# Optimization experiments

Hardware: AMD Instinct MI355X
Metric: run time of the kernel (lower is better)

Reference implementation:

```python
import jax, jax.numpy as jnp
import numpy as np

B, C_IN, H, W = 4, 256, 256, 256
L = 5000                 # candidate lines per image
N_PTS0, N_PTS1 = 32, 8   # sampled points per line, pooled points
DIM_LOI, DIM_FC = 128, 1024
N_OUT_LINE = 2500


def setup_inputs() -> dict:
    key = jax.random.key(0)
    ks = jax.random.split(key, 8)
    feature = jax.random.normal(ks[0], (B, C_IN, H, W), jnp.float32)
    # line endpoints in [0, 255) pixel coords (row, col)
    lines_in = jax.random.uniform(ks[1], (B, L, 2, 2), jnp.float32) * 255.0
    fc1_w = jax.random.normal(ks[2], (DIM_LOI, C_IN), jnp.float32) * 0.05
    fc1_b = jnp.zeros((DIM_LOI,), jnp.float32)
    w1 = jax.random.normal(ks[3], (DIM_FC, DIM_LOI * N_PTS1), jnp.float32) * 0.02
    b1 = jnp.zeros((DIM_FC,), jnp.float32)
    w2 = jax.random.normal(ks[4], (DIM_FC, DIM_FC), jnp.float32) * 0.02
    b2 = jnp.zeros((DIM_FC,), jnp.float32)
    w3 = jax.random.normal(ks[5], (4, DIM_FC), jnp.float32) * 0.02
    b3 = jnp.zeros((4,), jnp.float32)
    return dict(feature=feature, lines_in=lines_in, fc1_w=fc1_w, fc1_b=fc1_b,
                w1=w1, b1=b1, w2=w2, b2=b2, w3=w3, b3=b3)


def _bilinear_sample(xi, px, py):
    # xi: [C, H, W]; px, py: [P] float coords. Matches torch clamp(0, 255).
    px0 = jnp.clip(jnp.floor(px), 0.0, 255.0)
    py0 = jnp.clip(jnp.floor(py), 0.0, 255.0)
    px1 = jnp.clip(px0 + 1.0, 0.0, 255.0)
    py1 = jnp.clip(py0 + 1.0, 0.0, 255.0)
    px0l, py0l = px0.astype(jnp.int32), py0.astype(jnp.int32)
    px1l, py1l = px1.astype(jnp.int32), py1.astype(jnp.int32)
    xp = (xi[:, px0l, py0l] * (px1 - px) * (py1 - py)
          + xi[:, px1l, py0l] * (px - px0) * (py1 - py)
          + xi[:, px0l, py1l] * (px1 - px) * (py - py0)
          + xi[:, px1l, py1l] * (px - px0) * (py - py0))
    return xp  # [C, P]


def _select(p0, s0, m):
    # p0: [L,2,2], s0: [L,4], m: [L] bool. Threshold-masked, argsort by argmax
    # class (descending), cyclically padded to N_OUT_LINE.
    max_idx = jnp.argmax(s0, axis=1)
    sort_key = jnp.where(m, max_idx, -1)          # unmasked rows sink to the end
    order = jnp.argsort(-sort_key)                # stable, descending by class id
    cnt = m.sum()
    idxs = jnp.arange(N_OUT_LINE) % jnp.maximum(cnt, 1)
    sel = order[idxs]
    li = jnp.where(cnt > 0, p0[sel], jnp.zeros_like(p0[sel]))
    si = jnp.where(cnt > 0, s0[sel], jnp.zeros_like(s0[sel]))
    return li, si


def reference(feature, lines_in, fc1_w, fc1_b, w1, b1, w2, b2, w3, b3):
    # fc1: 1x1 conv -> [B, DIM_LOI, H, W]
    x = jnp.einsum('bchw,oc->bohw', feature, fc1_w) + fc1_b[None, :, None, None]

    # sample N_PTS0 points along each line: p0*lam + p1*(1-lam) - 0.5
    lam = jnp.linspace(0.0, 1.0, N_PTS0, dtype=jnp.float32)[:, None]  # [32,1]
    pts = lines_in[:, :, 0:1, :] * lam + lines_in[:, :, 1:2, :] * (1.0 - lam) - 0.5  # [B,L,32,2]
    px = pts[..., 0].reshape(B, -1)  # [B, L*32]
    py = pts[..., 1].reshape(B, -1)

    xp = jax.vmap(_bilinear_sample)(x, px, py)            # [B, C, L*32]
    xp = xp.reshape(B, DIM_LOI, L, N_PTS0).transpose(0, 2, 1, 3)  # [B, L, C, 32]

    # MaxPool1d(4, 4) over the point axis -> [B, L, C, 8]
    xp = xp.reshape(B, L, DIM_LOI, N_PTS1, N_PTS0 // N_PTS1).max(axis=-1)
    flat = xp.reshape(B, L, DIM_LOI * N_PTS1)

    # fc2 MLP: 1024 -> 1024 -> 1024 -> 4
    h = jax.nn.relu(jnp.einsum('blf,df->bld', flat, w1) + b1)
    h = jax.nn.relu(jnp.einsum('bld,ed->ble', h, w2) + b2)
    logits = jnp.einsum('ble,oe->blo', h, w3) + b3        # [B, L, 4]

    s = jax.nn.softmax(logits, axis=-1)
    mask = ((s[..., 1] > 0.25) | (s[..., 2] > 0.25) | (s[..., 3] > 0.25)) & (s[..., 0] < 0.25)

    lines_out, score_out = jax.vmap(_select)(lines_in, s, mask)
    return lines_out, score_out  # [B, 2500, 2, 2], [B, 2500, 4]
```

## Files before the change

### kernel.cpp

```cpp
#include <hip/hip_runtime.h>
#include <hip/hip_bf16.h>
#include <math.h>

#define BB 4
#define C_IN 256
#define HH 256
#define WW 256
#define LL 5000
#define N_PTS0 32
#define N_PTS1 8
#define DIM_LOI 128
#define DIM_FC 1024
#define N_OUT_LINE 2500
#define MM (BB * LL)
#define PIX (HH * WW)

typedef __attribute__((ext_vector_type(8))) short short8_t;
typedef __attribute__((ext_vector_type(4))) float float4v;

__device__ __forceinline__ short f2bf(float f) {
    union { float f; unsigned u; } c; c.f = f;
    unsigned u = c.u;
    u += 0x7FFFu + ((u >> 16) & 1u);
    return (short)(u >> 16);
}
__device__ __forceinline__ float bf2f(short h) {
    union { unsigned u; float f; } c; c.u = ((unsigned)(unsigned short)h) << 16;
    return c.f;
}

__global__ __launch_bounds__(256) void conv_mfma_kernel(
    const float* __restrict__ feat,
    const short* __restrict__ whi,
    const short* __restrict__ wlo,
    const float* __restrict__ bias,
    float* __restrict__ x)
{
    __shared__ short As_hi[128][40];
    __shared__ short As_lo[128][40];
    __shared__ short Ws_hi[128][40];
    __shared__ short Ws_lo[128][40];

    const int t  = threadIdx.x;
    const int m0 = blockIdx.x * 128;
    const int b  = m0 >> 16;
    const int p0 = m0 & (PIX - 1);
    const float* fb = feat + (size_t)b * C_IN * PIX + p0;

    const int w = t >> 6, lane = t & 63;
    const int wmb = (w >> 1) * 64, wnb = (w & 1) * 64;
    const int fr = lane & 15;
    const int koff = (lane >> 4) << 3;

    const int sp = t & 127;
    const int cg = t >> 7;

    float4v acc[4][4];
#pragma unroll
    for (int mi = 0; mi < 4; mi++)
#pragma unroll
        for (int ni = 0; ni < 4; ni++)
            acc[mi][ni] = (float4v){0.f, 0.f, 0.f, 0.f};

    for (int k0 = 0; k0 < C_IN; k0 += 32) {
#pragma unroll
        for (int i = 0; i < 2; i++) {
            int idx = t + (i << 8);
            int row = idx >> 2;
            int kc  = (idx & 3) << 3;
            *(int4*)&Ws_hi[row][kc] = *(const int4*)(whi + row * C_IN + k0 + kc);
            *(int4*)&Ws_lo[row][kc] = *(const int4*)(wlo + row * C_IN + k0 + kc);
        }
#pragma unroll
        for (int j = 0; j < 8; j++) {
            int c = cg * 16 + j * 2;
            float v0 = fb[(size_t)(k0 + c) * PIX + sp];
            float v1 = fb[(size_t)(k0 + c + 1) * PIX + sp];
            short h0 = f2bf(v0), h1 = f2bf(v1);
            short l0 = f2bf(v0 - bf2f(h0)), l1 = f2bf(v1 - bf2f(h1));
            *(unsigned*)&As_hi[sp][c] =
                (unsigned)(unsigned short)h0 | ((unsigned)(unsigned short)h1 << 16);
            *(unsigned*)&As_lo[sp][c] =
                (unsigned)(unsigned short)l0 | ((unsigned)(unsigned short)l1 << 16);
        }
        __syncthreads();

        short8_t ah[4], al[4];
#pragma unroll
        for (int mi = 0; mi < 4; mi++) {
            ah[mi] = *(const short8_t*)&As_hi[wmb + mi * 16 + fr][koff];
            al[mi] = *(const short8_t*)&As_lo[wmb + mi * 16 + fr][koff];
        }
#pragma unroll
        for (int ni = 0; ni < 4; ni++) {
            short8_t bh = *(const short8_t*)&Ws_hi[wnb + ni * 16 + fr][koff];
            short8_t bl = *(const short8_t*)&Ws_lo[wnb + ni * 16 + fr][koff];
#pragma unroll
            for (int mi = 0; mi < 4; mi++) {
                acc[mi][ni] = __builtin_amdgcn_mfma_f32_16x16x32_bf16(
                    ah[mi], bh, acc[mi][ni], 0, 0, 0);
                acc[mi][ni] = __builtin_amdgcn_mfma_f32_16x16x32_bf16(
                    al[mi], bh, acc[mi][ni], 0, 0, 0);
                acc[mi][ni] = __builtin_amdgcn_mfma_f32_16x16x32_bf16(
                    ah[mi], bl, acc[mi][ni], 0, 0, 0);
            }
        }
        __syncthreads();
    }

#pragma unroll
    for (int ni = 0; ni < 4; ni++) {
        int ncol = wnb + ni * 16 + fr;
        float bv = bias[ncol];
#pragma unroll
        for (int mi = 0; mi < 4; mi++) {
            int r0 = m0 + wmb + mi * 16 + ((lane >> 4) << 2);
#pragma unroll
            for (int i2 = 0; i2 < 4; i2++) {
                x[(size_t)(r0 + i2) * 128 + ncol] = acc[mi][ni][i2] + bv;
            }
        }
    }
}

__global__ __launch_bounds__(128) void sample_pool_kernel(
    const float* __restrict__ lines,
    const float* __restrict__ x,
    short* __restrict__ phi,
    short* __restrict__ plo)
{
    const int bl = blockIdx.x;
    const int b  = bl / LL;
    const int c  = threadIdx.x;
    const float* lp = lines + (size_t)bl * 4;
    const float p0r = lp[0], p0c = lp[1], p1r = lp[2], p1c = lp[3];
    const float* xb = x + (size_t)b * PIX * 128;

    short8_t vh, vl;
#pragma unroll
    for (int g = 0; g < 8; g++) {
        float mx = -INFINITY;
#pragma unroll
        for (int j = 0; j < 4; j++) {
            int tt = g * 4 + j;
            float lam = (float)((double)tt / 31.0);
            float px = p0r * lam + p1r * (1.0f - lam) - 0.5f;
            float py = p0c * lam + p1c * (1.0f - lam) - 0.5f;
            float px0 = fminf(fmaxf(floorf(px), 0.0f), 255.0f);
            float py0 = fminf(fmaxf(floorf(py), 0.0f), 255.0f);
            float px1 = fminf(px0 + 1.0f, 255.0f);
            float py1 = fminf(py0 + 1.0f, 255.0f);
            int ix0 = (int)px0, iy0 = (int)py0, ix1 = (int)px1, iy1 = (int)py1;
            float wx1 = px1 - px, wx0 = px - px0;
            float wy1 = py1 - py, wy0 = py - py0;
            float v00 = xb[(size_t)(ix0 * WW + iy0) * 128 + c];
            float v10 = xb[(size_t)(ix1 * WW + iy0) * 128 + c];
            float v01 = xb[(size_t)(ix0 * WW + iy1) * 128 + c];
            float v11 = xb[(size_t)(ix1 * WW + iy1) * 128 + c];
            float v = v00 * (wx1 * wy1) + v10 * (wx0 * wy1)
                    + v01 * (wx1 * wy0) + v11 * (wx0 * wy0);
            mx = fmaxf(mx, v);
        }
        short h = f2bf(mx);
        vh[g] = h;
        vl[g] = f2bf(mx - bf2f(h));
    }
    *(short8_t*)(phi + (size_t)bl * 1024 + c * 8) = vh;
    *(short8_t*)(plo + (size_t)bl * 1024 + c * 8) = vl;
}

__global__ __launch_bounds__(256) void split_kernel(
    const float* __restrict__ w, short* __restrict__ hi, short* __restrict__ lo)
{
    const int i = (blockIdx.x * 256 + threadIdx.x) * 4;
    float4 v = *(const float4*)(w + i);
    float vv[4] = {v.x, v.y, v.z, v.w};
    short4 h, l;
    short hs[4], ls[4];
#pragma unroll
    for (int j = 0; j < 4; j++) {
        hs[j] = f2bf(vv[j]);
        ls[j] = f2bf(vv[j] - bf2f(hs[j]));
    }
    h.x = hs[0]; h.y = hs[1]; h.z = hs[2]; h.w = hs[3];
    l.x = ls[0]; l.y = ls[1]; l.z = ls[2]; l.w = ls[3];
    *(short4*)(hi + i) = h;
    *(short4*)(lo + i) = l;
}

template <bool SPLIT_OUT>
__global__ __launch_bounds__(256) void gemm_bf16x3(
    const short* __restrict__ Ahi, const short* __restrict__ Alo,
    const short* __restrict__ Bhi, const short* __restrict__ Blo,
    const float* __restrict__ bias,
    float* __restrict__ Cf, short* __restrict__ Chi, short* __restrict__ Clo,
    int M)
{
    __shared__ short As_hi[128][40];
    __shared__ short As_lo[128][40];
    __shared__ short Bs_hi[128][40];
    __shared__ short Bs_lo[128][40];

    const int t = threadIdx.x;
    const int tileN = blockIdx.x & 7;
    const int tileM = blockIdx.x >> 3;
    const int m0 = tileM * 128, n0 = tileN * 128;
    const int w = t >> 6, lane = t & 63;
    const int wmb = (w >> 1) * 64, wnb = (w & 1) * 64;
    const int fr = lane & 15;
    const int koff = (lane >> 4) << 3;

    const short* gsrc[8];
    short* ldst[8];
#pragma unroll
    for (int i = 0; i < 8; i++) {
        int idx = t + (i << 8);
        int c = idx & 511;
        int row = c >> 2;
        int kc = (c & 3) << 3;
        int mat = idx >> 9;
        if (mat == 0) {
            int gr = min(m0 + row, M - 1);
            gsrc[i] = Ahi + (size_t)gr * 1024 + kc; ldst[i] = &As_hi[row][kc];
        } else if (mat == 1) {
            int gr = min(m0 + row, M - 1);
            gsrc[i] = Alo + (size_t)gr * 1024 + kc; ldst[i] = &As_lo[row][kc];
        } else if (mat == 2) {
            gsrc[i] = Bhi + (size_t)(n0 + row) * 1024 + kc; ldst[i] = &Bs_hi[row][kc];
        } else {
            gsrc[i] = Blo + (size_t)(n0 + row) * 1024 + kc; ldst[i] = &Bs_lo[row][kc];
        }
    }

    float4v acc[4][4];
#pragma unroll
    for (int mi = 0; mi < 4; mi++)
#pragma unroll
        for (int ni = 0; ni < 4; ni++)
            acc[mi][ni] = (float4v){0.f, 0.f, 0.f, 0.f};

    for (int k0 = 0; k0 < 1024; k0 += 32) {
#pragma unroll
        for (int i = 0; i < 8; i++) {
            int4 v = *(const int4*)(gsrc[i] + k0);
            *(int4*)(ldst[i]) = v;
        }
        __syncthreads();

        short8_t ah[4], al[4];
#pragma unroll
        for (int mi = 0; mi < 4; mi++) {
            ah[mi] = *(const short8_t*)&As_hi[wmb + mi * 16 + fr][koff];
            al[mi] = *(const short8_t*)&As_lo[wmb + mi * 16 + fr][koff];
        }
#pragma unroll
        for (int ni = 0; ni < 4; ni++) {
            short8_t bh = *(const short8_t*)&Bs_hi[wnb + ni * 16 + fr][koff];
            short8_t bl = *(const short8_t*)&Bs_lo[wnb + ni * 16 + fr][koff];
#pragma unroll
            for (int mi = 0; mi < 4; mi++) {
                acc[mi][ni] = __builtin_amdgcn_mfma_f32_16x16x32_bf16(
                    ah[mi], bh, acc[mi][ni], 0, 0, 0);
                acc[mi][ni] = __builtin_amdgcn_mfma_f32_16x16x32_bf16(
                    al[mi], bh, acc[mi][ni], 0, 0, 0);
                acc[mi][ni] = __builtin_amdgcn_mfma_f32_16x16x32_bf16(
                    ah[mi], bl, acc[mi][ni], 0, 0, 0);
            }
        }
        __syncthreads();
    }

#pragma unroll
    for (int ni = 0; ni < 4; ni++) {
        int ncol = n0 + wnb + ni * 16 + fr;
        float bv = bias[ncol];
#pragma unroll
        for (int mi = 0; mi < 4; mi++) {
            int r0 = m0 + wmb + mi * 16 + ((lane >> 4) << 2);
#pragma unroll
            for (int i2 = 0; i2 < 4; i2++) {
                int r = r0 + i2;
                if (r < M) {
                    float v = fmaxf(acc[mi][ni][i2] + bv, 0.0f);
                    if (SPLIT_OUT) {
                        short h = f2bf(v);
                        Chi[(size_t)r * 1024 + ncol] = h;
                        Clo[(size_t)r * 1024 + ncol] = f2bf(v - bf2f(h));
                    } else {
                        Cf[(size_t)r * 1024 + ncol] = v;
                    }
                }
            }
        }
    }
}

__global__ __launch_bounds__(256) void fc3_softmax_kernel(
    const float* __restrict__ h2, const float* __restrict__ w3,
    const float* __restrict__ b3, float* __restrict__ s, int* __restrict__ keys)
{
    const int m = blockIdx.x * 4 + (threadIdx.x >> 6);
    const int lane = threadIdx.x & 63;
    const float* hp = h2 + (size_t)m * DIM_FC;
    float a0 = 0.f, a1 = 0.f, a2 = 0.f, a3 = 0.f;
    for (int k = lane; k < DIM_FC; k += 64) {
        float hv = hp[k];
        a0 = fmaf(hv, w3[k], a0);
        a1 = fmaf(hv, w3[DIM_FC + k], a1);
        a2 = fmaf(hv, w3[2 * DIM_FC + k], a2);
        a3 = fmaf(hv, w3[3 * DIM_FC + k], a3);
    }
#pragma unroll
    for (int off = 32; off > 0; off >>= 1) {
        a0 += __shfl_down(a0, off, 64);
        a1 += __shfl_down(a1, off, 64);
        a2 += __shfl_down(a2, off, 64);
        a3 += __shfl_down(a3, off, 64);
    }
    if (lane == 0) {
        float l0 = a0 + b3[0], l1 = a1 + b3[1], l2 = a2 + b3[2], l3 = a3 + b3[3];
        float mxl = fmaxf(fmaxf(l0, l1), fmaxf(l2, l3));
        float e0 = expf(l0 - mxl), e1 = expf(l1 - mxl);
        float e2 = expf(l2 - mxl), e3 = expf(l3 - mxl);
        float inv = 1.0f / (e0 + e1 + e2 + e3);
        float s0 = e0 * inv, s1 = e1 * inv, s2 = e2 * inv, s3 = e3 * inv;
        float* sp = s + (size_t)m * 4;
        sp[0] = s0; sp[1] = s1; sp[2] = s2; sp[3] = s3;
        int best = 0; float bv = s0;
        if (s1 > bv) { best = 1; bv = s1; }
        if (s2 > bv) { best = 2; bv = s2; }
        if (s3 > bv) { best = 3; bv = s3; }
        bool msk = ((s1 > 0.25f) || (s2 > 0.25f) || (s3 > 0.25f)) && (s0 < 0.25f);
        keys[m] = msk ? best : -1;
    }
}

__global__ __launch_bounds__(64) void order_kernel(
    const int* __restrict__ keys, int* __restrict__ ord, int* __restrict__ cnts)
{
    const int b = blockIdx.x;
    const int lane = threadIdx.x;
    const int* kb = keys + b * LL;
    int c0 = 0, c1 = 0, c2 = 0, c3 = 0;
    for (int line = lane; line < LL; line += 64) {
        int k = kb[line];
        c0 += (k == 0); c1 += (k == 1); c2 += (k == 2); c3 += (k == 3);
    }
#pragma unroll
    for (int off = 32; off > 0; off >>= 1) {
        c0 += __shfl_down(c0, off, 64);
        c1 += __shfl_down(c1, off, 64);
        c2 += __shfl_down(c2, off, 64);
        c3 += __shfl_down(c3, off, 64);
    }
    int t0 = __shfl(c0, 0, 64), t1 = __shfl(c1, 0, 64);
    int t2 = __shfl(c2, 0, 64), t3 = __shfl(c3, 0, 64);
    if (lane == 0) cnts[b] = t0 + t1 + t2 + t3;
    int base[4];
    base[3] = 0; base[2] = t3; base[1] = t3 + t2; base[0] = t3 + t2 + t1;
    int run[4] = {0, 0, 0, 0};
    const unsigned long long below = (1ull << lane) - 1ull;
    int* ob = ord + b * LL;
    for (int s0 = 0; s0 < LL; s0 += 64) {
        int line = s0 + lane;
        int k = (line < LL) ? kb[line] : -2;
#pragma unroll
        for (int kk = 0; kk < 4; kk++) {
            unsigned long long mask = __ballot(k == kk);
            if (k == kk) {
                int pos = base[kk] + run[kk] + __popcll(mask & below);
                ob[pos] = line;
            }
            run[kk] += __popcll(mask);
        }
    }
}

__global__ __launch_bounds__(256) void fill_kernel(
    const float* __restrict__ lines, const float* __restrict__ s,
    const int* __restrict__ ord, const int* __restrict__ cnts,
    float* __restrict__ out)
{
    const int i = blockIdx.x * 256 + threadIdx.x;
    if (i >= BB * N_OUT_LINE) return;
    const int b = i / N_OUT_LINE;
    const int j = i % N_OUT_LINE;
    const int cnt = cnts[b];
    float4 lo = {0.f, 0.f, 0.f, 0.f}, sc = {0.f, 0.f, 0.f, 0.f};
    if (cnt > 0) {
        int line = ord[b * LL + (j % cnt)];
        lo = *(const float4*)(lines + ((size_t)b * LL + line) * 4);
        sc = *(const float4*)(s + ((size_t)b * LL + line) * 4);
    }
    *(float4*)(out + (size_t)i * 4) = lo;
    *(float4*)(out + (size_t)(BB * N_OUT_LINE) * 4 + (size_t)i * 4) = sc;
}

extern "C" void kernel_launch(void* const* d_in, const int* in_sizes, int n_in,
                              void* d_out, int out_size, void* d_ws, size_t ws_size,
                              hipStream_t stream) {
    (void)in_sizes; (void)n_in; (void)out_size; (void)ws_size;
    const float* feature = (const float*)d_in[0];
    const float* lines   = (const float*)d_in[1];
    const float* fc1_w   = (const float*)d_in[2];
    const float* fc1_b   = (const float*)d_in[3];
    const float* w1      = (const float*)d_in[4];
    const float* b1      = (const float*)d_in[5];
    const float* w2      = (const float*)d_in[6];
    const float* b2      = (const float*)d_in[7];
    const float* w3      = (const float*)d_in[8];
    const float* b3      = (const float*)d_in[9];
    float* out = (float*)d_out;

    float* x = (float*)d_ws;
    short* pooled_hi = (short*)(x + (size_t)BB * PIX * 128);
    short* pooled_lo = pooled_hi + (size_t)MM * DIM_FC;
    short* h1hi = (short*)x;
    short* h1lo = h1hi + (size_t)MM * DIM_FC;
    float* h2 = (float*)pooled_hi;
    short* w1hi = (short*)((char*)d_ws + 100u * 1024u * 1024u);
    short* w1lo = w1hi + DIM_FC * DIM_FC;
    short* w2hi = w1lo + DIM_FC * DIM_FC;
    short* w2lo = w2hi + DIM_FC * DIM_FC;
    float* s    = (float*)(pooled_lo + (size_t)MM * DIM_FC);
    int* keys   = (int*)(s + MM * 4);
    int* ord    = keys + MM;
    int* cnts   = ord + MM;
    short* fc1hi = (short*)(cnts + 64);
    short* fc1lo = fc1hi + DIM_LOI * C_IN;

    split_kernel<<<(DIM_LOI * C_IN) / 1024, 256, 0, stream>>>(fc1_w, fc1hi, fc1lo);
    conv_mfma_kernel<<<(BB * PIX) / 128, 256, 0, stream>>>(
        feature, fc1hi, fc1lo, fc1_b, x);
    sample_pool_kernel<<<MM, 128, 0, stream>>>(lines, x, pooled_hi, pooled_lo);
    split_kernel<<<DIM_FC * DIM_FC / 1024, 256, 0, stream>>>(w1, w1hi, w1lo);
    split_kernel<<<DIM_FC * DIM_FC / 1024, 256, 0, stream>>>(w2, w2hi, w2lo);

    const int mtiles = (MM + 127) / 128;
    gemm_bf16x3<true><<<mtiles * 8, 256, 0, stream>>>(
        pooled_hi, pooled_lo, w1hi, w1lo, b1, nullptr, h1hi, h1lo, MM);
    gemm_bf16x3<false><<<mtiles * 8, 256, 0, stream>>>(
        h1hi, h1lo, w2hi, w2lo, b2, h2, nullptr, nullptr, MM);

    fc3_softmax_kernel<<<MM / 4, 256, 0, stream>>>(h2, w3, b3, s, keys);
    order_kernel<<<BB, 64, 0, stream>>>(keys, ord, cnts);
    fill_kernel<<<(BB * N_OUT_LINE + 255) / 256, 256, 0, stream>>>(
        lines, s, ord, cnts, out);
}
```

Before: 966.3 us.

## Load GEMM tiles directly to LDS and group tile rasterization for L2 reuse

The bf16x3 GEMM now uses global_load_lds to move 16-byte chunks straight from global memory into LDS, with each wave loading one of the four operand matrices. This skips the register round-trip. Block indices are remapped so groups of 8 M-tiles share the same N-tile sweep, to improve L2 reuse of A and B, and out-of-range blocks exit early. The LDS padding is removed to fit the direct-load layout, which may raise bank conflicts on the fragment reads.

```diff
diff --git a/kernel.cpp b/kernel.cpp
--- a/kernel.cpp
+++ b/kernel.cpp
@@ -27,6 +27,12 @@
 __device__ __forceinline__ float bf2f(short h) {
     union { unsigned u; float f; } c; c.u = ((unsigned)(unsigned short)h) << 16;
     return c.f;
+}
+
+__device__ __forceinline__ void load_lds16(const void* g, void* l) {
+    __builtin_amdgcn_global_load_lds(
+        (const __attribute__((address_space(1))) void*)g,
+        (__attribute__((address_space(3))) void*)l, 16, 0, 0);
 }
 
 __global__ __launch_bounds__(256) void conv_mfma_kernel(
@@ -196,40 +202,29 @@
     float* __restrict__ Cf, short* __restrict__ Chi, short* __restrict__ Clo,
     int M)
 {
-    __shared__ short As_hi[128][40];
-    __shared__ short As_lo[128][40];
-    __shared__ short Bs_hi[128][40];
-    __shared__ short Bs_lo[128][40];
+    __shared__ short lds[4][128 * 32];
 
     const int t = threadIdx.x;
-    const int tileN = blockIdx.x & 7;
-    const int tileM = blockIdx.x >> 3;
+    const int blk = blockIdx.x;
+    const int tileM = (blk & 7) | ((blk >> 6) << 3);
+    const int tileN = (blk >> 3) & 7;
+    if (tileM * 128 >= M) return;
     const int m0 = tileM * 128, n0 = tileN * 128;
     const int w = t >> 6, lane = t & 63;
     const int wmb = (w >> 1) * 64, wnb = (w & 1) * 64;
     const int fr = lane & 15;
     const int koff = (lane >> 4) << 3;
 
-    const short* gsrc[8];
-    short* ldst[8];
+    const short* mats[4] = {Ahi, Alo, Bhi, Blo};
+    const short* gp[8];
+    void* lp[8];
 #pragma unroll
     for (int i = 0; i < 8; i++) {
-        int idx = t + (i << 8);
-        int c = idx & 511;
-        int row = c >> 2;
-        int kc = (c & 3) << 3;
-        int mat = idx >> 9;
-        if (mat == 0) {
-            int gr = min(m0 + row, M - 1);
-            gsrc[i] = Ahi + (size_t)gr * 1024 + kc; ldst[i] = &As_hi[row][kc];
-        } else if (mat == 1) {
-            int gr = min(m0 + row, M - 1);
-            gsrc[i] = Alo + (size_t)gr * 1024 + kc; ldst[i] = &As_lo[row][kc];
-        } else if (mat == 2) {
-            gsrc[i] = Bhi + (size_t)(n0 + row) * 1024 + kc; ldst[i] = &Bs_hi[row][kc];
-        } else {
-            gsrc[i] = Blo + (size_t)(n0 + row) * 1024 + kc; ldst[i] = &Bs_lo[row][kc];
-        }
+        int row = i * 16 + (lane >> 2);
+        int kc  = (lane & 3) * 8;
+        int grow = (w < 2) ? min(m0 + row, M - 1) : (n0 + row);
+        gp[i] = mats[w] + (size_t)grow * 1024 + kc;
+        lp[i] = &lds[w][i * 512 + lane * 8];
     }
 
     float4v acc[4][4];
@@ -242,21 +237,23 @@
     for (int k0 = 0; k0 < 1024; k0 += 32) {
 #pragma unroll
         for (int i = 0; i < 8; i++) {
-            int4 v = *(const int4*)(gsrc[i] + k0);
-            *(int4*)(ldst[i]) = v;
+            load_lds16(gp[i], lp[i]);
+            gp[i] += 32;
         }
         __syncthreads();
 
         short8_t ah[4], al[4];
 #pragma unroll
         for (int mi = 0; mi < 4; mi++) {
-            ah[mi] = *(const short8_t*)&As_hi[wmb + mi * 16 + fr][koff];
-            al[mi] = *(const short8_t*)&As_lo[wmb + mi * 16 + fr][koff];
+            int r = wmb + mi * 16 + fr;
+            ah[mi] = *(const short8_t*)&lds[0][r * 32 + koff];
+            al[mi] = *(const short8_t*)&lds[1][r * 32 + koff];
         }
 #pragma unroll
         for (int ni = 0; ni < 4; ni++) {
-            short8_t bh = *(const short8_t*)&Bs_hi[wnb + ni * 16 + fr][koff];
-            short8_t bl = *(const short8_t*)&Bs_lo[wnb + ni * 16 + fr][koff];
+            int r = wnb + ni * 16 + fr;
+            short8_t bh = *(const short8_t*)&lds[2][r * 32 + koff];
+            short8_t bl = *(const short8_t*)&lds[3][r * 32 + koff];
 #pragma unroll
             for (int mi = 0; mi < 4; mi++) {
                 acc[mi][ni] = __builtin_amdgcn_mfma_f32_16x16x32_bf16(
@@ -436,10 +433,10 @@
     split_kernel<<<DIM_FC * DIM_FC / 1024, 256, 0, stream>>>(w1, w1hi, w1lo);
     split_kernel<<<DIM_FC * DIM_FC / 1024, 256, 0, stream>>>(w2, w2hi, w2lo);
 
-    const int mtiles = (MM + 127) / 128;
-    gemm_bf16x3<true><<<mtiles * 8, 256, 0, stream>>>(
+    const int mgroups = (((MM + 127) / 128) + 7) / 8;
+    gemm_bf16x3<true><<<mgroups * 64, 256, 0, stream>>>(
         pooled_hi, pooled_lo, w1hi, w1lo, b1, nullptr, h1hi, h1lo, MM);
-    gemm_bf16x3<false><<<mtiles * 8, 256, 0, stream>>>(
+    gemm_bf16x3<false><<<mgroups * 64, 256, 0, stream>>>(
         h1hi, h1lo, w2hi, w2lo, b2, h2, nullptr, nullptr, MM);
 
     fc3_softmax_kernel<<<MM / 4, 256, 0, stream>>>(h2, w3, b3, s, keys);
```

After: 933.8 us. -3.4%, faster.
